# Optimization experiments

Measured on AMD Instinct MI355X. Metric: run time of the kernel, lower is better.

Reference implementation:

```python
import jax, jax.numpy as jnp
import numpy as np

NUM_EMBEDDINGS = 512
EMBEDDING_DIM = 64
COMMITMENT_COST = 0.25


def setup_inputs() -> dict:
    key = jax.random.key(0)
    k1, k2 = jax.random.split(key)
    inputs = jax.random.normal(k1, (8, 64, 32, 32, 32), dtype=jnp.float32)
    bound = 1.0 / NUM_EMBEDDINGS
    codebook = jax.random.uniform(
        k2, (NUM_EMBEDDINGS, EMBEDDING_DIM), dtype=jnp.float32,
        minval=-bound, maxval=bound)
    return {"inputs": inputs, "codebook": codebook}


def reference(inputs, codebook):
    # [B, C, D, H, W] -> [B, D, H, W, C]
    x = jnp.transpose(inputs, (0, 2, 3, 4, 1))
    input_shape = x.shape
    flat = x.reshape(-1, EMBEDDING_DIM)  # [N, C]

    # squared L2 distances to codebook: [N, K]
    distances = (
        jnp.sum(flat ** 2, axis=1, keepdims=True)
        + jnp.sum(codebook ** 2, axis=1)
        - 2.0 * flat @ codebook.T
    )
    encoding_indices = jnp.argmin(distances, axis=1)  # [N]
    quantized = codebook[encoding_indices].reshape(input_shape)

    sg = jax.lax.stop_gradient
    vq_loss = (
        jnp.mean((sg(quantized) - x) ** 2)
        + COMMITMENT_COST * jnp.mean((quantized - sg(x)) ** 2)
    )

    # straight-through estimator
    quantized_for_decoder = x + sg(quantized - x)
    # [B, D, H, W, C] -> [B, C, D, H, W]
    quantized_for_decoder = jnp.transpose(quantized_for_decoder, (0, 4, 1, 2, 3))
    return quantized_for_decoder, vq_loss, encoding_indices
```

## Files before the change

kernel.cpp:

```cpp
#include <hip/hip_runtime.h>

#define CC 64
#define NN 262144
#define NELEM 16777216
#define KK 512
#define CHUNK 64
#define NCHUNK 8
#define ROWS 128
#define TAU 4e-5f
#define CAP 28672

#define WS_CNT  0
#define WS_PART 64
#define WS_B    16448
#define WS_E1   18496
#define WS_E2   84032
#define WS_LIST 149568

typedef short short8 __attribute__((ext_vector_type(8)));
typedef float f32x4 __attribute__((ext_vector_type(4)));

__device__ __forceinline__ unsigned short bf16_rne(float x) {
    unsigned u = __float_as_uint(x);
    unsigned r = u + 0x7FFFu + ((u >> 16) & 1u);
    return (unsigned short)(r >> 16);
}
__device__ __forceinline__ float bf16_back(unsigned short h) {
    return __uint_as_float(((unsigned)h) << 16);
}

__global__ __launch_bounds__(256) void vq_prep(
    const float* __restrict__ cb, unsigned char* __restrict__ ws)
{
#pragma clang fp contract(off)
    const int k = blockIdx.x * 256 + threadIdx.x;
    if (k == 0) *(unsigned*)(ws + WS_CNT) = 0u;

    float e[CC];
    const float4* ep = (const float4*)(cb + k * CC);
    #pragma unroll
    for (int i = 0; i < 16; ++i) {
        float4 v = ep[i];
        e[4*i] = v.x; e[4*i+1] = v.y; e[4*i+2] = v.z; e[4*i+3] = v.w;
    }
    float q[8];
    #pragma unroll
    for (int j = 0; j < 8; ++j) q[j] = e[j] * e[j];
    #pragma unroll
    for (int i = 1; i < 8; ++i) {
        #pragma unroll
        for (int j = 0; j < 8; ++j) { float sq = e[8*i+j] * e[8*i+j]; q[j] = q[j] + sq; }
    }
    ((float*)(ws + WS_B))[k] = ((q[0]+q[1])+(q[2]+q[3]))+((q[4]+q[5])+(q[6]+q[7]));

    char* e1 = (char*)(ws + WS_E1);
    char* e2 = (char*)(ws + WS_E2);
    #pragma unroll
    for (int s = 0; s < 8; ++s) {
        short8 hi, lo;
        #pragma unroll
        for (int j = 0; j < 8; ++j) {
            float v = -2.0f * e[s*8 + j];
            unsigned short h = bf16_rne(v);
            hi[j] = (short)h;
            lo[j] = (short)bf16_rne(v - bf16_back(h));
        }
        const int off = k * 128 + ((s * 16) ^ ((k & 7) << 4));
        *(short8*)(e1 + off) = hi;
        *(short8*)(e2 + off) = lo;
    }
}

__global__ __launch_bounds__(256, 4) void vq_mfma(
    const float* __restrict__ in, const float* __restrict__ cb,
    unsigned char* __restrict__ ws,
    float* __restrict__ out_q, float* __restrict__ out_idx)
{
#pragma clang fp contract(off)
    __shared__ short  e1s[CHUNK * CC];
    __shared__ short  e2s[CHUNK * CC];
    __shared__ float  Bl_s[KK];
    __shared__ float  Al[ROWS];
    __shared__ int    idx_s[ROWS];
    __shared__ double red_s[256];

    const int tid  = threadIdx.x;
    const int lane = tid & 63;
    const int w    = tid >> 6;
    const int nb   = blockIdx.x * ROWS;
    const int bblk = nb >> 15;
    const float* xbase = in + ((size_t)bblk << 21) + (nb & 32767);

    if (tid < ROWS) {
        const float* xa = xbase + tid;
        float r[8];
        #pragma unroll
        for (int j = 0; j < 8; ++j) { float v = xa[(size_t)j << 15]; r[j] = v * v; }
        #pragma unroll
        for (int i = 1; i < 8; ++i) {
            #pragma unroll
            for (int j = 0; j < 8; ++j) {
                float v = xa[(size_t)(8*i + j) << 15];
                float sq = v * v;
                r[j] = r[j] + sq;
            }
        }
        Al[tid] = ((r[0]+r[1])+(r[2]+r[3]))+((r[4]+r[5])+(r[6]+r[7]));
    }
    {
        const float* wsB = (const float*)(ws + WS_B);
        Bl_s[tid] = wsB[tid]; Bl_s[tid + 256] = wsB[tid + 256];
    }
    __syncthreads();

    short8 a1[2][2], a2[2][2];
    {
        const int c0 = (lane >> 4) * 8;
        #pragma unroll
        for (int rt = 0; rt < 2; ++rt) {
            const float* xp = xbase + (w*32 + rt*16 + (lane & 15));
            #pragma unroll
            for (int j = 0; j < 8; ++j) {
                float v0 = xp[(size_t)(c0 + j) << 15];
                float v1 = xp[(size_t)(c0 + j + 32) << 15];
                unsigned short h0 = bf16_rne(v0), h1 = bf16_rne(v1);
                a1[rt][0][j] = (short)h0;
                a1[rt][1][j] = (short)h1;
                a2[rt][0][j] = (short)bf16_rne(v0 - bf16_back(h0));
                a2[rt][1][j] = (short)bf16_rne(v1 - bf16_back(h1));
            }
        }
    }

    float s1v[2][4], s2v[2][4];
    #pragma unroll
    for (int rt = 0; rt < 2; ++rt)
        #pragma unroll
        for (int r = 0; r < 4; ++r) { s1v[rt][r] = 3.4e38f; s2v[rt][r] = 3.4e38f; }

    const unsigned lanec = (unsigned)(lane & 15);

    for (int ch = 0; ch < NCHUNK; ++ch) {
        __syncthreads();
        {
            const char* s1p = (const char*)(ws + WS_E1 + ch * 8192) + tid * 16;
            const char* s2p = (const char*)(ws + WS_E2 + ch * 8192) + tid * 16;
            char* d1p = (char*)e1s + tid * 16;
            char* d2p = (char*)e2s + tid * 16;
            #pragma unroll
            for (int i = 0; i < 2; ++i) {
                __builtin_amdgcn_global_load_lds(
                    (const __attribute__((address_space(1))) unsigned int*)(s1p + i*4096),
                    (__attribute__((address_space(3))) unsigned int*)(d1p + i*4096), 16, 0, 0);
                __builtin_amdgcn_global_load_lds(
                    (const __attribute__((address_space(1))) unsigned int*)(s2p + i*4096),
                    (__attribute__((address_space(3))) unsigned int*)(d2p + i*4096), 16, 0, 0);
            }
        }
        __syncthreads();

        #pragma unroll
        for (int t16 = 0; t16 < 4; ++t16) {
            const int kt = ch*4 + t16;
            const int codeL = t16*16 + (lane & 15);
            const unsigned pc = ((unsigned)kt << 4) | lanec;
            short8 b1[2], b2[2];
            #pragma unroll
            for (int h = 0; h < 2; ++h) {
                const int byteoff = codeL*128 + (((4*h + (lane>>4)) * 16) ^ ((codeL & 7) << 4));
                b1[h] = *(const short8*)((const char*)e1s + byteoff);
                b2[h] = *(const short8*)((const char*)e2s + byteoff);
            }
            const float Bs = Bl_s[ch*CHUNK + codeL];
            #pragma unroll
            for (int rt = 0; rt < 2; ++rt) {
                f32x4 acc = {Bs, Bs, Bs, Bs};
                acc = __builtin_amdgcn_mfma_f32_16x16x32_bf16(a1[rt][0], b1[0], acc, 0, 0, 0);
                acc = __builtin_amdgcn_mfma_f32_16x16x32_bf16(a1[rt][1], b1[1], acc, 0, 0, 0);
                acc = __builtin_amdgcn_mfma_f32_16x16x32_bf16(a2[rt][0], b1[0], acc, 0, 0, 0);
                acc = __builtin_amdgcn_mfma_f32_16x16x32_bf16(a2[rt][1], b1[1], acc, 0, 0, 0);
                acc = __builtin_amdgcn_mfma_f32_16x16x32_bf16(a1[rt][0], b2[0], acc, 0, 0, 0);
                acc = __builtin_amdgcn_mfma_f32_16x16x32_bf16(a1[rt][1], b2[1], acc, 0, 0, 0);
                #pragma unroll
                for (int r = 0; r < 4; ++r) {
                    float dp = __uint_as_float((__float_as_uint(acc[r]) & 0xFFFFFE00u) | pc);
                    s2v[rt][r] = __builtin_amdgcn_fmed3f(dp, s1v[rt][r], s2v[rt][r]);
                    s1v[rt][r] = __builtin_fminf(s1v[rt][r], dp);
                }
            }
        }
    }

    unsigned* cnt  = (unsigned*)(ws + WS_CNT);
    unsigned* list = (unsigned*)(ws + WS_LIST);
    double lsum = 0.0;
    #pragma unroll
    for (int rt = 0; rt < 2; ++rt) {
        #pragma unroll
        for (int r = 0; r < 4; ++r) {
            float s1 = s1v[rt][r], s2 = s2v[rt][r];
            #pragma unroll
            for (int off = 1; off < 16; off <<= 1) {
                float s1o = __shfl_xor(s1, off);
                float s2o = __shfl_xor(s2, off);
                s2 = __builtin_fminf(__builtin_fminf(s2, s2o), __builtin_fmaxf(s1, s1o));
                s1 = __builtin_fminf(s1, s1o);
            }
            if ((lane & 15) == 0) {
                const int rl = w*32 + rt*16 + (lane>>4)*4 + r;
                const int code = (int)(__float_as_uint(s1) & 511u);
                out_idx[nb + rl] = (float)code;
                idx_s[rl] = code;
                if (s2 - s1 < TAU) {
                    unsigned pos = atomicAdd(cnt, 1u);
                    if (pos < CAP) list[pos] = (unsigned)(nb + rl);
                }
                lsum += (double)(Al[rl] + s1);
            }
        }
    }
    red_s[tid] = lsum;
    __syncthreads();

    {
        const int row = tid >> 1, c0 = (tid & 1) << 5;
        const int myidx = idx_s[row];
        const float4* cbr = (const float4*)cb + myidx*16 + (c0 >> 2);
        float* qp = out_q + ((size_t)bblk << 21) + (nb & 32767) + row;
        #pragma unroll
        for (int cg = 0; cg < 8; ++cg) {
            float4 ev = cbr[cg];
            qp[(size_t)(c0 + 4*cg + 0) << 15] = ev.x;
            qp[(size_t)(c0 + 4*cg + 1) << 15] = ev.y;
            qp[(size_t)(c0 + 4*cg + 2) << 15] = ev.z;
            qp[(size_t)(c0 + 4*cg + 3) << 15] = ev.w;
        }
    }
    for (int off = 128; off; off >>= 1) {
        if (tid < off) red_s[tid] += red_s[tid + off];
        __syncthreads();
    }
    if (tid == 0) ((double*)(ws + WS_PART))[blockIdx.x] = red_s[0];
}

__global__ __launch_bounds__(256, 2) void vq_recheck(
    const float* __restrict__ in, const float* __restrict__ cb,
    unsigned char* __restrict__ ws,
    float* __restrict__ out_q, float* __restrict__ out_loss,
    float* __restrict__ out_idx)
{
#pragma clang fp contract(off)
    __shared__ float xs[4][CC];
    const int tid  = threadIdx.x;
    const int lane = tid & 63;
    const int w    = tid >> 6;

    if (blockIdx.x == 0 && w == 0) {
        const double* partials = (const double*)(ws + WS_PART);
        double p = 0.0;
        #pragma unroll
        for (int j = 0; j < 32; ++j) p += partials[lane*32 + j];
        #pragma unroll
        for (int off = 1; off < 64; off <<= 1) p += __shfl_xor(p, off);
        if (lane == 0) *out_loss = (float)(1.25 * p / (double)NELEM);
    }

    const unsigned m = *(const unsigned*)(ws + WS_CNT);
    const unsigned* list = (const unsigned*)(ws + WS_LIST);
    const float* Bw = (const float*)(ws + WS_B);
    const unsigned total = (m <= CAP) ? m : NN;

    for (unsigned i = blockIdx.x * 4 + w; i < total; i += gridDim.x * 4) {
        const unsigned n = (m <= CAP) ? list[i] : i;
        const int oldidx = (int)out_idx[n];
        const float* xp = in + ((size_t)(n >> 15) << 21) + (n & 32767);

        xs[w][lane] = xp[(size_t)lane << 15];

        float r0[8];
        #pragma unroll
        for (int j = 0; j < 8; ++j) { float v = xs[w][j]; r0[j] = v * v; }
        #pragma unroll
        for (int ii = 1; ii < 8; ++ii) {
            #pragma unroll
            for (int j = 0; j < 8; ++j) { float v = xs[w][8*ii + j]; float sq = v * v; r0[j] = r0[j] + sq; }
        }
        const float A = ((r0[0]+r0[1])+(r0[2]+r0[3]))+((r0[4]+r0[5])+(r0[6]+r0[7]));

        float cacc[8];
        #pragma unroll
        for (int jj = 0; jj < 8; ++jj) cacc[jj] = 0.f;
        const float4* cb4 = (const float4*)cb;
        #pragma unroll 1
        for (int c4 = 0; c4 < 16; ++c4) {
            float4 x4 = *(const float4*)&xs[w][c4 * 4];
            #pragma unroll
            for (int jj = 0; jj < 8; ++jj) {
                float4 ev = cb4[(size_t)(jj*64 + lane) * 16 + c4];
                cacc[jj] = __builtin_fmaf(x4.x, ev.x, cacc[jj]);
                cacc[jj] = __builtin_fmaf(x4.y, ev.y, cacc[jj]);
                cacc[jj] = __builtin_fmaf(x4.z, ev.z, cacc[jj]);
                cacc[jj] = __builtin_fmaf(x4.w, ev.w, cacc[jj]);
            }
        }

        float best = 3.4e38f; int bk = 0;
        #pragma unroll
        for (int jj = 0; jj < 8; ++jj) {
            const int k = jj*64 + lane;
            const float t1 = A + Bw[k];
            const float t2 = 2.0f * cacc[jj];
            const float D = t1 - t2;
            if (D < best) { best = D; bk = k; }
        }
        #pragma unroll
        for (int off = 1; off < 64; off <<= 1) {
            float bo = __shfl_xor(best, off);
            int   ko = __shfl_xor(bk, off);
            if (bo < best || (bo == best && ko < bk)) { best = bo; bk = ko; }
        }
        if (bk != oldidx) {
            if (lane == 0) out_idx[n] = (float)bk;
            out_q[((size_t)(n >> 15) << 21) + ((size_t)lane << 15) + (n & 32767)] = cb[bk*CC + lane];
        }
    }
}

extern "C" void kernel_launch(void* const* d_in, const int* in_sizes, int n_in,
                              void* d_out, int out_size, void* d_ws, size_t ws_size,
                              hipStream_t stream) {
    const float* in = (const float*)d_in[0];
    const float* cb = (const float*)d_in[1];
    float* out      = (float*)d_out;
    float* out_q    = out;
    float* out_loss = out + NELEM;
    float* out_idx  = out + NELEM + 1;
    unsigned char* ws = (unsigned char*)d_ws;

    vq_prep<<<2, 256, 0, stream>>>(cb, ws);
    vq_mfma<<<NN / ROWS, 256, 0, stream>>>(in, cb, ws, out_q, out_idx);
    vq_recheck<<<1024, 256, 0, stream>>>(in, cb, ws, out_q, out_loss, out_idx);
}
```

Baseline: 113.9 us.

## Load codebook fragments straight from global into registers with double buffering

Drops the LDS staging of the bf16 hi/lo codebook chunks and the barriers around it. Each wave now reads its B fragments directly from global memory (L2/L1-cached, shared by all blocks) into registers, using a two-deep software pipeline so the next tile's loads overlap the current tile's MFMAs. The XOR swizzle in the prep layout is removed because LDS bank conflicts no longer apply. The trade-off is more global/L1 traffic per wave and more registers in exchange for less LDS use and fewer synchronisations.

```diff
diff --git a/kernel.cpp b/kernel.cpp
--- a/kernel.cpp
+++ b/kernel.cpp
@@ -4,9 +4,8 @@
 #define NN 262144
 #define NELEM 16777216
 #define KK 512
-#define CHUNK 64
-#define NCHUNK 8
 #define ROWS 128
+#define NBLK (NN/ROWS)
 #define TAU 4e-5f
 #define CAP 28672
 
@@ -65,7 +64,7 @@
             hi[j] = (short)h;
             lo[j] = (short)bf16_rne(v - bf16_back(h));
         }
-        const int off = k * 128 + ((s * 16) ^ ((k & 7) << 4));
+        const int off = k * 128 + s * 16;
         *(short8*)(e1 + off) = hi;
         *(short8*)(e2 + off) = lo;
     }
@@ -77,8 +76,6 @@
     float* __restrict__ out_q, float* __restrict__ out_idx)
 {
 #pragma clang fp contract(off)
-    __shared__ short  e1s[CHUNK * CC];
-    __shared__ short  e2s[CHUNK * CC];
     __shared__ float  Bl_s[KK];
     __shared__ float  Al[ROWS];
     __shared__ int    idx_s[ROWS];
@@ -111,7 +108,6 @@
         const float* wsB = (const float*)(ws + WS_B);
         Bl_s[tid] = wsB[tid]; Bl_s[tid + 256] = wsB[tid + 256];
     }
-    __syncthreads();
 
     short8 a1[2][2], a2[2][2];
     {
@@ -131,6 +127,7 @@
             }
         }
     }
+    __syncthreads();
 
     float s1v[2][4], s2v[2][4];
     #pragma unroll
@@ -140,56 +137,50 @@
 
     const unsigned lanec = (unsigned)(lane & 15);
 
-    for (int ch = 0; ch < NCHUNK; ++ch) {
-        __syncthreads();
-        {
-            const char* s1p = (const char*)(ws + WS_E1 + ch * 8192) + tid * 16;
-            const char* s2p = (const char*)(ws + WS_E2 + ch * 8192) + tid * 16;
-            char* d1p = (char*)e1s + tid * 16;
-            char* d2p = (char*)e2s + tid * 16;
-            #pragma unroll
-            for (int i = 0; i < 2; ++i) {
-                __builtin_amdgcn_global_load_lds(
-                    (const __attribute__((address_space(1))) unsigned int*)(s1p + i*4096),
-                    (__attribute__((address_space(3))) unsigned int*)(d1p + i*4096), 16, 0, 0);
-                __builtin_amdgcn_global_load_lds(
-                    (const __attribute__((address_space(1))) unsigned int*)(s2p + i*4096),
-                    (__attribute__((address_space(3))) unsigned int*)(d2p + i*4096), 16, 0, 0);
-            }
-        }
-        __syncthreads();
-
-        #pragma unroll
-        for (int t16 = 0; t16 < 4; ++t16) {
-            const int kt = ch*4 + t16;
-            const int codeL = t16*16 + (lane & 15);
-            const unsigned pc = ((unsigned)kt << 4) | lanec;
-            short8 b1[2], b2[2];
-            #pragma unroll
-            for (int h = 0; h < 2; ++h) {
-                const int byteoff = codeL*128 + (((4*h + (lane>>4)) * 16) ^ ((codeL & 7) << 4));
-                b1[h] = *(const short8*)((const char*)e1s + byteoff);
-                b2[h] = *(const short8*)((const char*)e2s + byteoff);
-            }
-            const float Bs = Bl_s[ch*CHUNK + codeL];
-            #pragma unroll
-            for (int rt = 0; rt < 2; ++rt) {
-                f32x4 acc = {Bs, Bs, Bs, Bs};
-                acc = __builtin_amdgcn_mfma_f32_16x16x32_bf16(a1[rt][0], b1[0], acc, 0, 0, 0);
-                acc = __builtin_amdgcn_mfma_f32_16x16x32_bf16(a1[rt][1], b1[1], acc, 0, 0, 0);
-                acc = __builtin_amdgcn_mfma_f32_16x16x32_bf16(a2[rt][0], b1[0], acc, 0, 0, 0);
-                acc = __builtin_amdgcn_mfma_f32_16x16x32_bf16(a2[rt][1], b1[1], acc, 0, 0, 0);
-                acc = __builtin_amdgcn_mfma_f32_16x16x32_bf16(a1[rt][0], b2[0], acc, 0, 0, 0);
-                acc = __builtin_amdgcn_mfma_f32_16x16x32_bf16(a1[rt][1], b2[1], acc, 0, 0, 0);
-                #pragma unroll
-                for (int r = 0; r < 4; ++r) {
-                    float dp = __uint_as_float((__float_as_uint(acc[r]) & 0xFFFFFE00u) | pc);
-                    s2v[rt][r] = __builtin_amdgcn_fmed3f(dp, s1v[rt][r], s2v[rt][r]);
-                    s1v[rt][r] = __builtin_fminf(s1v[rt][r], dp);
-                }
-            }
-        }
-    }
+    const char* e1g = (const char*)(ws + WS_E1) + (lane & 15) * 128 + (lane >> 4) * 16;
+    const char* e2g = (const char*)(ws + WS_E2) + (lane & 15) * 128 + (lane >> 4) * 16;
+
+    #define LOADB(B1, B2, kt) {                                   \
+        const int off_ = (kt) * 2048;                             \
+        B1[0] = *(const short8*)(e1g + off_);                     \
+        B1[1] = *(const short8*)(e1g + off_ + 64);                \
+        B2[0] = *(const short8*)(e2g + off_);                     \
+        B2[1] = *(const short8*)(e2g + off_ + 64); }
+
+    auto MFMAT = [&](const short8* B1, const short8* B2, int kt) {
+        const float Bs = Bl_s[kt*16 + (lane & 15)];
+        const unsigned pc = ((unsigned)kt << 4) | lanec;
+        #pragma unroll
+        for (int rt = 0; rt < 2; ++rt) {
+            f32x4 acc = {Bs, Bs, Bs, Bs};
+            acc = __builtin_amdgcn_mfma_f32_16x16x32_bf16(a1[rt][0], B1[0], acc, 0, 0, 0);
+            acc = __builtin_amdgcn_mfma_f32_16x16x32_bf16(a1[rt][1], B1[1], acc, 0, 0, 0);
+            acc = __builtin_amdgcn_mfma_f32_16x16x32_bf16(a2[rt][0], B1[0], acc, 0, 0, 0);
+            acc = __builtin_amdgcn_mfma_f32_16x16x32_bf16(a2[rt][1], B1[1], acc, 0, 0, 0);
+            acc = __builtin_amdgcn_mfma_f32_16x16x32_bf16(a1[rt][0], B2[0], acc, 0, 0, 0);
+            acc = __builtin_amdgcn_mfma_f32_16x16x32_bf16(a1[rt][1], B2[1], acc, 0, 0, 0);
+            #pragma unroll
+            for (int r = 0; r < 4; ++r) {
+                float dp = __uint_as_float((__float_as_uint(acc[r]) & 0xFFFFFE00u) | pc);
+                s2v[rt][r] = __builtin_amdgcn_fmed3f(dp, s1v[rt][r], s2v[rt][r]);
+                s1v[rt][r] = __builtin_fminf(s1v[rt][r], dp);
+            }
+        }
+    };
+
+    {
+        short8 pA1[2], pA2[2], pB1[2], pB2[2];
+        LOADB(pA1, pA2, 0);
+        #pragma unroll
+        for (int kt2 = 0; kt2 < 16; ++kt2) {
+            const int k0 = 2*kt2;
+            LOADB(pB1, pB2, k0 + 1);
+            MFMAT(pA1, pA2, k0);
+            if (kt2 < 15) LOADB(pA1, pA2, k0 + 2);
+            MFMAT(pB1, pB2, k0 + 1);
+        }
+    }
+    #undef LOADB
 
     unsigned* cnt  = (unsigned*)(ws + WS_CNT);
     unsigned* list = (unsigned*)(ws + WS_LIST);
@@ -338,6 +329,6 @@
     unsigned char* ws = (unsigned char*)d_ws;
 
     vq_prep<<<2, 256, 0, stream>>>(cb, ws);
-    vq_mfma<<<NN / ROWS, 256, 0, stream>>>(in, cb, ws, out_q, out_idx);
+    vq_mfma<<<NBLK, 256, 0, stream>>>(in, cb, ws, out_q, out_idx);
     vq_recheck<<<1024, 256, 0, stream>>>(in, cb, ws, out_q, out_loss, out_idx);
 }
```

Measured after the change: 362.0 us. 218% more time.
